# Kernel tuning notes

Hardware: AMD Instinct MI355X
Metric: run time of the kernel (lower is better)

## Reference

```python
import jax, jax.numpy as jnp
import numpy as np

L, C, H, DH, S, N, B = 12, 768, 12, 64, 2, 577, 1
ALT_START, ROPE_START = 0, 0
OUT_LAYERS = (2, 5, 8, 11)
EPS = 1e-6


def _ln(x, w, b):
    m = jnp.mean(x, axis=-1, keepdims=True)
    v = jnp.var(x, axis=-1, keepdims=True)
    return (x - m) * jax.lax.rsqrt(v + EPS) * w + b


def _rms(x, w):
    return x * jax.lax.rsqrt(jnp.mean(x * x, axis=-1, keepdims=True) + EPS) * w


def _rot_half(x):
    h = x.shape[-1] // 2
    return jnp.concatenate([-x[..., h:], x[..., :h]], axis=-1)


def _rope(t, cos, sin):
    # t: [Bf, H, N, DH]; cos/sin: [N, DH] split into y/x halves
    h = t.shape[-1] // 2
    tv, th = t[..., :h], t[..., h:]
    cy, cx = cos[..., :h], cos[..., h:]
    sy, sx = sin[..., :h], sin[..., h:]
    return jnp.concatenate([tv * cy + _rot_half(tv) * sy,
                            th * cx + _rot_half(th) * sx], axis=-1)


def _block(xf, cos, sin, kv, p):
    (qkv_w, qkv_b, qn, kn, pw, pb, g1, g2,
     n1w, n1b, n2w, n2b, f1w, f1b, f2w, f2b) = p
    Bf, Nn, Cc = xf.shape
    h = _ln(xf, n1w, n1b)
    qkv = (jnp.einsum('bnc,oc->bno', h, qkv_w) + qkv_b)
    qkv = qkv.reshape(Bf, Nn, 3, H, DH).transpose(2, 0, 3, 1, 4)
    q, k, v = qkv[0], qkv[1], qkv[2]
    q, k = _rms(q, qn), _rms(k, kn)
    q, k = _rope(q, cos, sin), _rope(k, cos, sin)
    bias = ((1.0 - kv) * (-10000.0))[:, None, None, :]
    scores = jnp.einsum('bhqd,bhkd->bhqk', q, k) / np.sqrt(DH) + bias
    attn = jax.nn.softmax(scores, axis=-1)
    o = jnp.einsum('bhqk,bhkd->bhqd', attn, v).transpose(0, 2, 1, 3).reshape(Bf, Nn, Cc)
    o = jnp.einsum('bnc,oc->bno', o, pw) + pb
    xf = xf + g1 * o
    h2 = _ln(xf, n2w, n2b)
    m = jax.nn.gelu(jnp.einsum('bnc,oc->bno', h2, f1w) + f1b, approximate=False)
    m = jnp.einsum('bnd,od->bno', m, f2w) + f2b
    return xf + g2 * m


def _forward(x, rope_cos_local, rope_sin_local, rope_cos_global, rope_sin_global,
             key_valid_local, key_valid_global, camera_token,
             qkv_w, qkv_b, q_norm_w, k_norm_w, proj_w, proj_b,
             ls1_gamma, ls2_gamma, norm1_w, norm1_b, norm2_w, norm2_b,
             fc1_w, fc1_b, fc2_w, fc2_b, final_norm_w, final_norm_b):
    Bb, Ss, Nn, Cc = x.shape
    stacked = (qkv_w, qkv_b, q_norm_w, k_norm_w, proj_w, proj_b, ls1_gamma,
               ls2_gamma, norm1_w, norm1_b, norm2_w, norm2_b, fc1_w, fc1_b,
               fc2_w, fc2_b)
    local_x = x
    outputs = []
    cam_token_out = None
    max_out = max(OUT_LAYERS)
    for i in range(L):
        if i == ALT_START:
            ref = jnp.broadcast_to(camera_token[:, :1], (Bb, 1, Cc))
            src = jnp.broadcast_to(camera_token[:, 1:], (Bb, Ss - 1, Cc))
            x = x.at[:, :, 0].set(jnp.concatenate([ref, src], axis=1))
        p = tuple(a[i] for a in stacked)
        is_global = (i % 2 == 1)  # alt_start == 0
        if is_global:
            xf = x.reshape(Bb, Ss * Nn, Cc)
            xf = _block(xf, rope_cos_global, rope_sin_global, key_valid_global, p)
            x = xf.reshape(Bb, Ss, Nn, Cc)
        else:
            xf = x.reshape(Bb * Ss, Nn, Cc)
            xf = _block(xf, rope_cos_local, rope_sin_local, key_valid_local, p)
            x = xf.reshape(Bb, Ss, Nn, Cc)
            local_x = x
        if i in OUT_LAYERS:
            out_x = jnp.concatenate([local_x, x], axis=-1)  # cat_token=True
            outputs.append(out_x)
            if i == max_out:
                cam_token_out = out_x[:, :, 0]
    processed = []
    for o in outputs:
        o = jnp.concatenate([o[..., :Cc], _ln(o[..., Cc:], final_norm_w, final_norm_b)], axis=-1)
        o = o[..., 1:, :]  # drop cam/cls token (num_register_tokens=0)
        processed.append(o)
    return (processed[0], processed[1], processed[2], processed[3], cam_token_out)


def setup_inputs() -> dict:
    key = jax.random.key(0)
    ks = iter(jax.random.split(key, 40))
    rn = lambda sh, s=0.02: jax.random.normal(next(ks), sh, dtype=jnp.float32) * s
    two_pi = 2.0 * np.pi
    ang_l = jax.random.uniform(next(ks), (N, DH), dtype=jnp.float32) * two_pi
    ang_g = jax.random.uniform(next(ks), (S * N, DH), dtype=jnp.float32) * two_pi
    kv_l = (jax.random.uniform(next(ks), (B * S, N)) > 0.1).astype(jnp.float32)
    kv_g = (jax.random.uniform(next(ks), (B, S * N)) > 0.1).astype(jnp.float32)
    return {
        'x': rn((B, S, N, C), 1.0),
        'rope_cos_local': jnp.cos(ang_l), 'rope_sin_local': jnp.sin(ang_l),
        'rope_cos_global': jnp.cos(ang_g), 'rope_sin_global': jnp.sin(ang_g),
        'key_valid_local': kv_l, 'key_valid_global': kv_g,
        'camera_token': rn((1, 2, C)),
        'qkv_w': rn((L, 3 * C, C)), 'qkv_b': rn((L, 3 * C)),
        'q_norm_w': jnp.ones((L, DH), jnp.float32),
        'k_norm_w': jnp.ones((L, DH), jnp.float32),
        'proj_w': rn((L, C, C)), 'proj_b': rn((L, C)),
        'ls1_gamma': rn((L, C), 0.1), 'ls2_gamma': rn((L, C), 0.1),
        'norm1_w': jnp.ones((L, C), jnp.float32), 'norm1_b': jnp.zeros((L, C), jnp.float32),
        'norm2_w': jnp.ones((L, C), jnp.float32), 'norm2_b': jnp.zeros((L, C), jnp.float32),
        'fc1_w': rn((L, 4 * C, C)), 'fc1_b': rn((L, 4 * C)),
        'fc2_w': rn((L, C, 4 * C)), 'fc2_b': rn((L, C)),
        'final_norm_w': jnp.ones((C,), jnp.float32),
        'final_norm_b': jnp.zeros((C,), jnp.float32),
    }


def reference(x, rope_cos_local, rope_sin_local, rope_cos_global, rope_sin_global,
              key_valid_local, key_valid_global, camera_token,
              qkv_w, qkv_b, q_norm_w, k_norm_w, proj_w, proj_b,
              ls1_gamma, ls2_gamma, norm1_w, norm1_b, norm2_w, norm2_b,
              fc1_w, fc1_b, fc2_w, fc2_b, final_norm_w, final_norm_b):
    return _forward(x, rope_cos_local, rope_sin_local, rope_cos_global, rope_sin_global,
                    key_valid_local, key_valid_global, camera_token,
                    qkv_w, qkv_b, q_norm_w, k_norm_w, proj_w, proj_b,
                    ls1_gamma, ls2_gamma, norm1_w, norm1_b, norm2_w, norm2_b,
                    fc1_w, fc1_b, fc2_w, fc2_b, final_norm_w, final_norm_b)
```

## Files before the change

kernel.cpp:

```cpp
#include <hip/hip_runtime.h>
#include <hip/hip_bf16.h>
#include <math.h>

typedef __hip_bfloat16 bf16;
typedef __attribute__((ext_vector_type(4))) float floatx4;
typedef __attribute__((ext_vector_type(8))) short shortx8;

#define T_TOK 1154
#define C_DIM 768
#define H_HEADS 12
#define NLOC 577
#define OUT_PER 1769472

#define NQ  1769472ull
#define NP  589824ull
#define NF1 2359296ull
#define NF2 2359296ull
#define NWTOT 7077888ull
#define WQ  0ull
#define WP  1769472ull
#define WF1 2359296ull
#define WF2 4718592ull

static __device__ __forceinline__ float b2f(bf16 v) { return __bfloat162float(v); }
static __device__ __forceinline__ bf16 f2b(float v) { return __float2bfloat16(v); }

static __device__ __forceinline__ void gload16(const bf16* g, short* l) {
    __builtin_amdgcn_global_load_lds(
        (__attribute__((address_space(1))) void*)(void*)g,
        (__attribute__((address_space(3))) void*)(void*)l, 16, 0, 0);
}

__global__ void k_init(const float* __restrict__ xin, const float* __restrict__ cam,
                       float* __restrict__ xF, int total) {
    int idx = blockIdx.x * 256 + threadIdx.x;
    if (idx >= total) return;
    int t = idx / C_DIM, c = idx - t * C_DIM;
    int s = t / NLOC, n = t - s * NLOC;
    float v = (n == 0) ? cam[s * C_DIM + c] : xin[idx];
    xF[idx] = v;
}

__global__ void k_cast(const float* __restrict__ src, bf16* __restrict__ dst, int total) {
    int idx = blockIdx.x * 256 + threadIdx.x;
    if (idx < total) dst[idx] = f2b(src[idx]);
}

__global__ __launch_bounds__(256) void k_wconv3(
    const float* __restrict__ wq, const float* __restrict__ wp,
    const float* __restrict__ wf1, const float* __restrict__ wf2,
    bf16* __restrict__ dst) {
    int typ = blockIdx.y, layer = blockIdx.z;
    size_t cnt, off;
    const float* srcb;
    if (typ == 0)      { cnt = NQ;  off = WQ;  srcb = wq; }
    else if (typ == 1) { cnt = NP;  off = WP;  srcb = wp; }
    else if (typ == 2) { cnt = NF1; off = WF1; srcb = wf1; }
    else               { cnt = NF2; off = WF2; srcb = wf2; }
    size_t e = ((size_t)blockIdx.x * 256 + threadIdx.x) * 8;
    if (e >= cnt) return;
    const float* src = srcb + (size_t)layer * cnt + e;
    bf16* d = dst + (size_t)layer * NWTOT + off + e;
    float4 a = *(const float4*)(src);
    float4 b = *(const float4*)(src + 4);
    bf16 pk[8];
    pk[0] = f2b(a.x); pk[1] = f2b(a.y); pk[2] = f2b(a.z); pk[3] = f2b(a.w);
    pk[4] = f2b(b.x); pk[5] = f2b(b.y); pk[6] = f2b(b.z); pk[7] = f2b(b.w);
    *(shortx8*)d = *(shortx8*)pk;
}

__global__ __launch_bounds__(256) void k_ln(const float* __restrict__ xF,
                                            const float* __restrict__ w, const float* __restrict__ b,
                                            bf16* __restrict__ out) {
    int t = blockIdx.x;
    const float* xr = xF + (size_t)t * C_DIM;
    float s = 0.f, s2 = 0.f;
    for (int c = threadIdx.x; c < C_DIM; c += 256) { float v = xr[c]; s += v; s2 += v * v; }
    __shared__ float red[8];
    for (int o = 32; o; o >>= 1) { s += __shfl_xor(s, o, 64); s2 += __shfl_xor(s2, o, 64); }
    int wv = threadIdx.x >> 6;
    if ((threadIdx.x & 63) == 0) { red[wv] = s; red[4 + wv] = s2; }
    __syncthreads();
    s = red[0] + red[1] + red[2] + red[3];
    s2 = red[4] + red[5] + red[6] + red[7];
    float mean = s * (1.0f / C_DIM);
    float var = s2 * (1.0f / C_DIM) - mean * mean;
    if (var < 0.f) var = 0.f;
    float inv = rsqrtf(var + 1e-6f);
    bf16* orow = out + (size_t)t * C_DIM;
    for (int c = threadIdx.x; c < C_DIM; c += 256) {
        float v = (xr[c] - mean) * inv * w[c] + b[c];
        orow[c] = f2b(v);
    }
}

template<int BM, int BN, int MODE>
__global__ __launch_bounds__(256) void k_gemmT(
    const bf16* __restrict__ A, const bf16* __restrict__ Bt,
    const float* __restrict__ bias, const float* __restrict__ gamma,
    bf16* __restrict__ outB, float* __restrict__ xio,
    int M, int N, int K, int mB, int kS) {
    constexpr int FM = BM / 32;
    constexpr int FN = BN / 32;
    __shared__ short At[2][BM * 64];
    __shared__ short Bs[2][BN * 64];
    int nwg = gridDim.x;
    int lid = blockIdx.x;
    int qd = nwg >> 3, rm = nwg & 7;
    int xcd = lid & 7, pos = lid >> 3;
    int lid2 = (xcd < rm ? xcd * (qd + 1) : rm * (qd + 1) + (xcd - rm) * qd) + pos;
    int mI = lid2 % mB;
    int rest = lid2 / mB;
    int nB = N / BN;
    int nI = rest % nB;
    int kI = rest / nB;
    int m0 = mI * BM, n0 = nI * BN;
    int Ksub = K / kS;
    int kOff = kI * Ksub;
    int tid = threadIdx.x;
    int w = tid >> 6, lane = tid & 63;
    int lr = lane & 15, lq = lane >> 4;
    int wm = w & 1, wn = w >> 1;
    int srow = tid >> 3;
    int schk = tid & 7;
    floatx4 acc[FM][FN] = {};

    auto stage = [&](int buf, int k0) {
        #pragma unroll
        for (int j = 0; j < BM / 32; j++) {
            int r = j * 32 + srow;
            int ar = m0 + r; if (ar >= M) ar = M - 1;
            int gs = schk ^ (r & 7);
            gload16(A + (size_t)ar * K + kOff + k0 + gs * 8, &At[buf][r * 64 + schk * 8]);
        }
        #pragma unroll
        for (int j = 0; j < BN / 32; j++) {
            int r = j * 32 + srow;
            int gs = schk ^ (r & 7);
            gload16(Bt + (size_t)(n0 + r) * K + kOff + k0 + gs * 8, &Bs[buf][r * 64 + schk * 8]);
        }
    };

    int nt = Ksub / 64;
    stage(0, 0);
    __syncthreads();
    int cur = 0;
    int rx = lr & 7;
    for (int t = 0; t < nt; ++t) {
        if (t + 1 < nt) stage(cur ^ 1, (t + 1) * 64);
        #pragma unroll
        for (int kk = 0; kk < 2; kk++) {
            shortx8 af[FM], bg[FN];
            #pragma unroll
            for (int mi = 0; mi < FM; mi++) {
                int rowl = wm * (BM / 2) + mi * 16 + lr;
                af[mi] = *(const shortx8*)&At[cur][rowl * 64 + ((kk * 4 + lq) ^ rx) * 8];
            }
            #pragma unroll
            for (int ni = 0; ni < FN; ni++) {
                int rowl = wn * (BN / 2) + ni * 16 + lr;
                bg[ni] = *(const shortx8*)&Bs[cur][rowl * 64 + ((kk * 4 + lq) ^ rx) * 8];
            }
            #pragma unroll
            for (int mi = 0; mi < FM; mi++)
                #pragma unroll
                for (int ni = 0; ni < FN; ni++)
                    acc[mi][ni] = __builtin_amdgcn_mfma_f32_16x16x32_bf16(af[mi], bg[ni], acc[mi][ni], 0, 0, 0);
        }
        __syncthreads();
        cur ^= 1;
    }

    #pragma unroll
    for (int mi = 0; mi < FM; mi++) {
        #pragma unroll
        for (int ni = 0; ni < FN; ni++) {
            int cc = n0 + wn * (BN / 2) + ni * 16 + lr;
            #pragma unroll
            for (int rg = 0; rg < 4; rg++) {
                int rr = m0 + wm * (BM / 2) + mi * 16 + lq * 4 + rg;
                if (rr < M) {
                    float u = acc[mi][ni][rg];
                    if (MODE == 2) {
                        u += (kI == 0) ? bias[cc] : 0.f;
                        float contrib = gamma[cc] * u;
                        if (kS > 1) atomicAdd(&xio[(size_t)rr * N + cc], contrib);
                        else        xio[(size_t)rr * N + cc] += contrib;
                    } else if (MODE == 1) {
                        u += bias[cc];
                        float g = 0.5f * u * (1.0f + erff(u * 0.70710678118f));
                        outB[(size_t)rr * N + cc] = f2b(g);
                    } else {
                        u += bias[cc];
                        outB[(size_t)rr * N + cc] = f2b(u);
                    }
                }
            }
        }
    }
}

__global__ __launch_bounds__(256) void k_gemmQKV(
    const bf16* __restrict__ A, const bf16* __restrict__ Bt,
    const float* __restrict__ bias,
    const float* __restrict__ qnw, const float* __restrict__ knw,
    const float* __restrict__ ctab, const float* __restrict__ stab, int posMod,
    bf16* __restrict__ qh, bf16* __restrict__ kh, bf16* __restrict__ vh,
    int M, int K) {
    constexpr int BM = 64, BN = 64, FM = 2, FN = 2;
    const int N = 2304, mB = 19;
    __shared__ short At[2][BM * 64];
    __shared__ short Bs[2][BN * 64];
    __shared__ float ssqS[2][64];
    int nwg = gridDim.x;
    int lid = blockIdx.x;
    int qd = nwg >> 3, rm = nwg & 7;
    int xcd = lid & 7, pos = lid >> 3;
    int lid2 = (xcd < rm ? xcd * (qd + 1) : rm * (qd + 1) + (xcd - rm) * qd) + pos;
    int mI = lid2 % mB;
    int nI = lid2 / mB;
    int m0 = mI * BM, n0 = nI * BN;
    int tid = threadIdx.x;
    int w = tid >> 6, lane = tid & 63;
    int lr = lane & 15, lq = lane >> 4;
    int wm = w & 1, wn = w >> 1;
    int srow = tid >> 3, schk = tid & 7;
    floatx4 acc[FM][FN] = {};

    auto stage = [&](int buf, int k0) {
        #pragma unroll
        for (int j = 0; j < BM / 32; j++) {
            int r = j * 32 + srow;
            int ar = m0 + r; if (ar >= M) ar = M - 1;
            int gs = schk ^ (r & 7);
            gload16(A + (size_t)ar * K + k0 + gs * 8, &At[buf][r * 64 + schk * 8]);
        }
        #pragma unroll
        for (int j = 0; j < BN / 32; j++) {
            int r = j * 32 + srow;
            int gs = schk ^ (r & 7);
            gload16(Bt + (size_t)(n0 + r) * K + k0 + gs * 8, &Bs[buf][r * 64 + schk * 8]);
        }
    };

    int nt = K / 64;
    stage(0, 0);
    __syncthreads();
    int cur = 0;
    int rx = lr & 7;
    for (int t = 0; t < nt; ++t) {
        if (t + 1 < nt) stage(cur ^ 1, (t + 1) * 64);
        #pragma unroll
        for (int kk = 0; kk < 2; kk++) {
            shortx8 af[FM], bg[FN];
            #pragma unroll
            for (int mi = 0; mi < FM; mi++) {
                int rowl = wm * 32 + mi * 16 + lr;
                af[mi] = *(const shortx8*)&At[cur][rowl * 64 + ((kk * 4 + lq) ^ rx) * 8];
            }
            #pragma unroll
            for (int ni = 0; ni < FN; ni++) {
                int rowl = wn * 32 + ni * 16 + lr;
                bg[ni] = *(const shortx8*)&Bs[cur][rowl * 64 + ((kk * 4 + lq) ^ rx) * 8];
            }
            #pragma unroll
            for (int mi = 0; mi < FM; mi++)
                #pragma unroll
                for (int ni = 0; ni < FN; ni++)
                    acc[mi][ni] = __builtin_amdgcn_mfma_f32_16x16x32_bf16(af[mi], bg[ni], acc[mi][ni], 0, 0, 0);
        }
        __syncthreads();
        cur ^= 1;
    }

    int tile6 = n0 >> 6;
    int typ = tile6 / 12;
    int hh = tile6 - typ * 12;
    float u[FM][FN][4];
    #pragma unroll
    for (int mi = 0; mi < FM; mi++)
        #pragma unroll
        for (int ni = 0; ni < FN; ni++) {
            int cc = n0 + wn * 32 + ni * 16 + lr;
            #pragma unroll
            for (int rg = 0; rg < 4; rg++) u[mi][ni][rg] = acc[mi][ni][rg] + bias[cc];
        }

    if (typ == 2) {
        #pragma unroll
        for (int mi = 0; mi < FM; mi++)
            #pragma unroll
            for (int rg = 0; rg < 4; rg++) {
                int rr = m0 + wm * 32 + mi * 16 + lq * 4 + rg;
                if (rr < M) {
                    #pragma unroll
                    for (int ni = 0; ni < FN; ni++) {
                        int d = wn * 32 + ni * 16 + lr;
                        vh[((size_t)hh * T_TOK + rr) * 64 + d] = f2b(u[mi][ni][rg]);
                    }
                }
            }
        return;
    }

    float sq[FM][4];
    #pragma unroll
    for (int mi = 0; mi < FM; mi++)
        #pragma unroll
        for (int rg = 0; rg < 4; rg++) {
            float s = u[mi][0][rg] * u[mi][0][rg] + u[mi][1][rg] * u[mi][1][rg];
            for (int o = 1; o < 16; o <<= 1) s += __shfl_xor(s, o, 16);
            sq[mi][rg] = s;
        }
    if (lr == 0) {
        #pragma unroll
        for (int mi = 0; mi < FM; mi++)
            #pragma unroll
            for (int rg = 0; rg < 4; rg++)
                ssqS[wn][wm * 32 + mi * 16 + lq * 4 + rg] = sq[mi][rg];
    }
    __syncthreads();
    const float* wt = (typ == 0) ? qnw : knw;
    bf16* dstp = (typ == 0) ? qh : kh;
    int d0 = wn * 32 + lr;
    int d1 = d0 + 16;
    float w0 = wt[d0], w1 = wt[d1];
    #pragma unroll
    for (int mi = 0; mi < FM; mi++) {
        #pragma unroll
        for (int rg = 0; rg < 4; rg++) {
            int rowl = wm * 32 + mi * 16 + lq * 4 + rg;
            int rr = m0 + rowl;
            if (rr >= M) continue;
            float ssq = ssqS[0][rowl] + ssqS[1][rowl];
            float rinv = rsqrtf(ssq * (1.0f / 64.0f) + 1e-6f);
            float n0v = u[mi][0][rg] * rinv * w0;
            float n1v = u[mi][1][rg] * rinv * w1;
            int p = (rr >= posMod) ? rr - posMod : rr;
            float c0 = ctab[p * 64 + d0], s0 = stab[p * 64 + d0];
            float c1 = ctab[p * 64 + d1], s1 = stab[p * 64 + d1];
            float o0 = n0v * c0 - n1v * s0;
            float o1 = n1v * c1 + n0v * s1;
            size_t ob = ((size_t)hh * T_TOK + rr) * 64;
            dstp[ob + d0] = f2b(o0);
            dstp[ob + d1] = f2b(o1);
        }
    }
}

__global__ __launch_bounds__(256) void k_attn2(
    const bf16* __restrict__ qh, const bf16* __restrict__ kh, const bf16* __restrict__ vh,
    const float* __restrict__ mask, bf16* __restrict__ out, int nk) {
    __shared__ short Ks[64 * 72];
    __shared__ short Vs[64 * 72];
    __shared__ short Ps[4][16 * 72];
    __shared__ float bias_s[64];
    int h = blockIdx.y;
    int base = blockIdx.z * nk;
    int tid = threadIdx.x;
    int wv = tid >> 6, lane = tid & 63;
    int lr = lane & 15, lq = lane >> 4;
    int q0 = blockIdx.x * 64 + wv * 16;
    shortx8 qf[2];
    {
        int qr = q0 + lr; if (qr >= nk) qr = nk - 1;
        const bf16* qp = qh + ((size_t)h * T_TOK + base + qr) * 64 + lq * 8;
        qf[0] = *(const shortx8*)(qp);
        qf[1] = *(const shortx8*)(qp + 32);
    }
    int kKr[2], kSeg[2], vKr[2], vSeg[2];
    #pragma unroll
    for (int c = 0; c < 2; c++) {
        int idx = tid + c * 256;
        kKr[c] = idx >> 3; kSeg[c] = idx & 7;
        vKr[c] = idx & 63; vSeg[c] = idx >> 6;
    }
    shortx8 kpre[2], vpre[2];
    float bpre = 0.f;
    auto prefetch = [&](int kbase) {
        #pragma unroll
        for (int c = 0; c < 2; c++) {
            int gk = kbase + kKr[c];
            shortx8 kv = {};
            if (gk < nk) kv = *(const shortx8*)(kh + ((size_t)h * T_TOK + base + gk) * 64 + kSeg[c] * 8);
            kpre[c] = kv;
            int gv = kbase + vKr[c];
            shortx8 vv = {};
            if (gv < nk) vv = *(const shortx8*)(vh + ((size_t)h * T_TOK + base + gv) * 64 + vSeg[c] * 8);
            vpre[c] = vv;
        }
        if (tid < 64) {
            int gk = kbase + tid;
            bpre = (gk < nk) ? (1.0f - mask[base + gk]) * -10000.0f : -30000.0f;
        }
    };
    float mrow[4] = {-3.0e38f, -3.0e38f, -3.0e38f, -3.0e38f};
    float lrow[4] = {0.f, 0.f, 0.f, 0.f};
    floatx4 accO[4] = {};
    short* pbuf = &Ps[wv][0];
    int nkt = (nk + 63) >> 6;
    prefetch(0);
    for (int kt0 = 0; kt0 < nkt; kt0++) {
        __syncthreads();
        #pragma unroll
        for (int c = 0; c < 2; c++) {
            *(shortx8*)&Ks[kKr[c] * 72 + kSeg[c] * 8] = kpre[c];
            bf16* vb = (bf16*)&vpre[c];
            #pragma unroll
            for (int j = 0; j < 8; j++)
                Vs[(vSeg[c] * 8 + j) * 72 + vKr[c]] = *(short*)&vb[j];
        }
        if (tid < 64) bias_s[tid] = bpre;
        if (kt0 + 1 < nkt) prefetch((kt0 + 1) * 64);
        __syncthreads();
        floatx4 s[4];
        #pragma unroll
        for (int nt = 0; nt < 4; nt++) {
            floatx4 accS = {};
            shortx8 k0 = *(const shortx8*)&Ks[(nt * 16 + lr) * 72 + lq * 8];
            shortx8 k1 = *(const shortx8*)&Ks[(nt * 16 + lr) * 72 + 32 + lq * 8];
            accS = __builtin_amdgcn_mfma_f32_16x16x32_bf16(qf[0], k0, accS, 0, 0, 0);
            accS = __builtin_amdgcn_mfma_f32_16x16x32_bf16(qf[1], k1, accS, 0, 0, 0);
            s[nt] = accS;
        }
        float tmax[4] = {-3.0e38f, -3.0e38f, -3.0e38f, -3.0e38f};
        #pragma unroll
        for (int nt = 0; nt < 4; nt++) {
            float bv = bias_s[nt * 16 + lr];
            #pragma unroll
            for (int rg = 0; rg < 4; rg++) {
                float sv = s[nt][rg] * 0.125f + bv;
                s[nt][rg] = sv;
                tmax[rg] = fmaxf(tmax[rg], sv);
            }
        }
        #pragma unroll
        for (int rg = 0; rg < 4; rg++) {
            for (int o = 1; o < 16; o <<= 1) tmax[rg] = fmaxf(tmax[rg], __shfl_xor(tmax[rg], o, 16));
        }
        float fac[4], tsum[4] = {0.f, 0.f, 0.f, 0.f};
        #pragma unroll
        for (int rg = 0; rg < 4; rg++) {
            float mn = fmaxf(mrow[rg], tmax[rg]);
            fac[rg] = __expf(mrow[rg] - mn);
            mrow[rg] = mn;
        }
        #pragma unroll
        for (int nt = 0; nt < 4; nt++) {
            #pragma unroll
            for (int rg = 0; rg < 4; rg++) {
                float e = __expf(s[nt][rg] - mrow[rg]);
                s[nt][rg] = e;
                tsum[rg] += e;
            }
        }
        #pragma unroll
        for (int rg = 0; rg < 4; rg++) {
            for (int o = 1; o < 16; o <<= 1) tsum[rg] += __shfl_xor(tsum[rg], o, 16);
            lrow[rg] = lrow[rg] * fac[rg] + tsum[rg];
        }
        #pragma unroll
        for (int dt = 0; dt < 4; dt++)
            #pragma unroll
            for (int rg = 0; rg < 4; rg++) accO[dt][rg] *= fac[rg];
        #pragma unroll
        for (int nt = 0; nt < 4; nt++) {
            #pragma unroll
            for (int rg = 0; rg < 4; rg++) {
                bf16 pv = f2b(s[nt][rg]);
                pbuf[(lq * 4 + rg) * 72 + nt * 16 + lr] = *(short*)&pv;
            }
        }
        #pragma unroll
        for (int ks = 0; ks < 2; ks++) {
            shortx8 pf = *(const shortx8*)&pbuf[lr * 72 + ks * 32 + lq * 8];
            #pragma unroll
            for (int dt = 0; dt < 4; dt++) {
                shortx8 vf = *(const shortx8*)&Vs[(dt * 16 + lr) * 72 + ks * 32 + lq * 8];
                accO[dt] = __builtin_amdgcn_mfma_f32_16x16x32_bf16(pf, vf, accO[dt], 0, 0, 0);
            }
        }
    }
    float invl[4];
    #pragma unroll
    for (int rg = 0; rg < 4; rg++) invl[rg] = 1.0f / lrow[rg];
    #pragma unroll
    for (int rg = 0; rg < 4; rg++) {
        int qr = q0 + lq * 4 + rg;
        if (qr < nk) {
            bf16* orow = out + (size_t)(base + qr) * C_DIM + h * 64 + lr;
            #pragma unroll
            for (int dt = 0; dt < 4; dt++)
                orow[dt * 16] = f2b(accO[dt][rg] * invl[rg]);
        }
    }
}

__global__ __launch_bounds__(256) void k_output(
    const float* __restrict__ xF, const bf16* __restrict__ lxB,
    const float* __restrict__ fw, const float* __restrict__ fb, float* __restrict__ dst) {
    int b = blockIdx.x;
    int s = b / 576, nn = b - s * 576;
    int t = s * NLOC + nn + 1;
    const float* xr = xF + (size_t)t * C_DIM;
    float sum = 0.f, s2 = 0.f;
    for (int c = threadIdx.x; c < C_DIM; c += 256) { float v = xr[c]; sum += v; s2 += v * v; }
    __shared__ float red[8];
    for (int o = 32; o; o >>= 1) { sum += __shfl_xor(sum, o, 64); s2 += __shfl_xor(s2, o, 64); }
    if ((threadIdx.x & 63) == 0) { red[threadIdx.x >> 6] = sum; red[4 + (threadIdx.x >> 6)] = s2; }
    __syncthreads();
    sum = red[0] + red[1] + red[2] + red[3];
    s2 = red[4] + red[5] + red[6] + red[7];
    float mean = sum * (1.0f / C_DIM);
    float var = s2 * (1.0f / C_DIM) - mean * mean;
    if (var < 0.f) var = 0.f;
    float inv = rsqrtf(var + 1e-6f);
    float* orow = dst + (size_t)b * 1536;
    const bf16* lr = lxB + (size_t)t * C_DIM;
    for (int c = threadIdx.x; c < C_DIM; c += 256) {
        orow[c] = b2f(lr[c]);
        float v = (xr[c] - mean) * inv * fw[c] + fb[c];
        orow[768 + c] = v;
    }
}

__global__ void k_cam(const float* __restrict__ xF, const bf16* __restrict__ lxB,
                      float* __restrict__ dst) {
    for (int idx = threadIdx.x; idx < 2 * 1536; idx += 256) {
        int s = idx / 1536, c = idx - s * 1536;
        int t = s * NLOC;
        float v = (c < 768) ? b2f(lxB[(size_t)t * 768 + c]) : xF[(size_t)t * 768 + (c - 768)];
        dst[idx] = v;
    }
}

extern "C" void kernel_launch(void* const* d_in, const int* in_sizes, int n_in,
                              void* d_out, int out_size, void* d_ws, size_t ws_size,
                              hipStream_t stream) {
    const float* xin  = (const float*)d_in[0];
    const float* rcl  = (const float*)d_in[1];
    const float* rsl  = (const float*)d_in[2];
    const float* rcg  = (const float*)d_in[3];
    const float* rsg  = (const float*)d_in[4];
    const float* kvl  = (const float*)d_in[5];
    const float* kvg  = (const float*)d_in[6];
    const float* cam  = (const float*)d_in[7];
    const float* qkvw = (const float*)d_in[8];
    const float* qkvb = (const float*)d_in[9];
    const float* qnw  = (const float*)d_in[10];
    const float* knw  = (const float*)d_in[11];
    const float* pw   = (const float*)d_in[12];
    const float* pb   = (const float*)d_in[13];
    const float* ls1  = (const float*)d_in[14];
    const float* ls2  = (const float*)d_in[15];
    const float* n1w  = (const float*)d_in[16];
    const float* n1b  = (const float*)d_in[17];
    const float* n2w  = (const float*)d_in[18];
    const float* n2b  = (const float*)d_in[19];
    const float* f1w  = (const float*)d_in[20];
    const float* f1b  = (const float*)d_in[21];
    const float* f2w  = (const float*)d_in[22];
    const float* f2b_ = (const float*)d_in[23];
    const float* fnw  = (const float*)d_in[24];
    const float* fnb  = (const float*)d_in[25];

    char* ws = (char*)d_ws;
    const size_t TC = (size_t)T_TOK * C_DIM;
    float* xF  = (float*)ws; ws += TC * 4;
    bf16* bufA = (bf16*)ws;  ws += (size_t)T_TOK * 3072 * 2;
    bf16* qhb  = (bf16*)ws;  ws += TC * 2;
    bf16* khb  = (bf16*)ws;  ws += TC * 2;
    bf16* vhb  = (bf16*)ws;  ws += TC * 2;
    bf16* hbuf = (bf16*)ws;  ws += TC * 2;
    bf16* lxB  = (bf16*)ws;  ws += TC * 2;
    bf16* wAll = (bf16*)ws;
    size_t usedBase = (size_t)(ws - (char*)d_ws);
    bool bigW = ws_size >= usedBase + 12ull * NWTOT * 2ull;
    (void)n_in; (void)in_sizes; (void)out_size;

    float* out_b = (float*)d_out;

    k_init<<<(int)((TC + 255) / 256), 256, 0, stream>>>(xin, cam, xF, (int)TC);
    if (bigW)
        k_wconv3<<<dim3(1152, 4, 12), 256, 0, stream>>>(qkvw, pw, f1w, f2w, wAll);

    int outIdx = 0;
    for (int i = 0; i < 12; i++) {
        bool isGlobal = (i & 1);
        bf16* wL;
        if (bigW) {
            wL = wAll + (size_t)i * NWTOT;
        } else {
            k_wconv3<<<dim3(1152, 4, 1), 256, 0, stream>>>(
                qkvw + (size_t)i * NQ, pw + (size_t)i * NP,
                f1w + (size_t)i * NF1, f2w + (size_t)i * NF2, wAll);
            wL = wAll;
        }
        k_ln<<<T_TOK, 256, 0, stream>>>(xF, n1w + (size_t)i * 768, n1b + (size_t)i * 768, hbuf);
        k_gemmQKV<<<684, 256, 0, stream>>>(hbuf, wL + WQ,
            qkvb + (size_t)i * 2304,
            qnw + (size_t)i * 64, knw + (size_t)i * 64,
            isGlobal ? rcg : rcl, isGlobal ? rsg : rsl, isGlobal ? 1154 : 577,
            qhb, khb, vhb, T_TOK, 768);
        if (isGlobal)
            k_attn2<<<dim3(19, 12, 1), 256, 0, stream>>>(qhb, khb, vhb, kvg, hbuf, 1154);
        else
            k_attn2<<<dim3(10, 12, 2), 256, 0, stream>>>(qhb, khb, vhb, kvl, hbuf, 577);
        k_gemmT<64, 64, 2><<<456, 256, 0, stream>>>(hbuf, wL + WP,
            pb + (size_t)i * 768, ls1 + (size_t)i * 768, nullptr, xF, T_TOK, 768, 768, 19, 2);
        k_ln<<<T_TOK, 256, 0, stream>>>(xF, n2w + (size_t)i * 768, n2b + (size_t)i * 768, hbuf);
        k_gemmT<64, 64, 1><<<912, 256, 0, stream>>>(hbuf, wL + WF1,
            f1b + (size_t)i * 3072, nullptr, bufA, nullptr, T_TOK, 3072, 768, 19, 1);
        k_gemmT<64, 64, 2><<<912, 256, 0, stream>>>(bufA, wL + WF2,
            f2b_ + (size_t)i * 768, ls2 + (size_t)i * 768, nullptr, xF, T_TOK, 768, 3072, 19, 4);

        if (i == 2 || i == 4 || i == 8 || i == 10)
            k_cast<<<(int)((TC + 255) / 256), 256, 0, stream>>>(xF, lxB, (int)TC);

        if (i == 2 || i == 5 || i == 8 || i == 11) {
            k_output<<<1152, 256, 0, stream>>>(xF, lxB, fnw, fnb, out_b + (size_t)outIdx * OUT_PER);
            if (i == 11)
                k_cam<<<1, 256, 0, stream>>>(xF, lxB, out_b + 4ull * OUT_PER);
            outIdx++;
        }
    }
}
```

Before: 1.783 ms.

## Replace atomic split-K residual adds with partial buffers folded into layernorm

The proj and FC2 GEMMs now write their split-K partials into a two-slice float buffer instead of doing atomicAdd or read-modify-write into the residual. The next layernorm, or a new fold kernel at output layers, adds the partials into the residual stream and can also cast it to bf16. FC2 split-K drops from four slices to two, halving its grid. The weight conversion kernel also handles 16 elements per thread. This removes atomic traffic at the cost of extra partial-buffer reads and writes and a less parallel FC2.

```diff
diff --git a/kernel.cpp b/kernel.cpp
--- a/kernel.cpp
+++ b/kernel.cpp
@@ -41,9 +41,21 @@
     xF[idx] = v;
 }
 
-__global__ void k_cast(const float* __restrict__ src, bf16* __restrict__ dst, int total) {
-    int idx = blockIdx.x * 256 + threadIdx.x;
-    if (idx < total) dst[idx] = f2b(src[idx]);
+__global__ __launch_bounds__(256) void k_fold(
+    float* __restrict__ xF, const float* __restrict__ p0, const float* __restrict__ p1,
+    bf16* __restrict__ lxB, int doCast, int total4) {
+    int i = blockIdx.x * 256 + threadIdx.x;
+    if (i >= total4) return;
+    float4 x = ((float4*)xF)[i];
+    float4 a = ((const float4*)p0)[i];
+    float4 b = ((const float4*)p1)[i];
+    x.x += a.x + b.x; x.y += a.y + b.y; x.z += a.z + b.z; x.w += a.w + b.w;
+    ((float4*)xF)[i] = x;
+    if (doCast) {
+        bf16 pk[4];
+        pk[0] = f2b(x.x); pk[1] = f2b(x.y); pk[2] = f2b(x.z); pk[3] = f2b(x.w);
+        *(short4*)(lxB + (size_t)i * 4) = *(short4*)pk;
+    }
 }
 
 __global__ __launch_bounds__(256) void k_wconv3(
@@ -57,26 +69,39 @@
     else if (typ == 1) { cnt = NP;  off = WP;  srcb = wp; }
     else if (typ == 2) { cnt = NF1; off = WF1; srcb = wf1; }
     else               { cnt = NF2; off = WF2; srcb = wf2; }
-    size_t e = ((size_t)blockIdx.x * 256 + threadIdx.x) * 8;
+    size_t e = ((size_t)blockIdx.x * 256 + threadIdx.x) * 16;
     if (e >= cnt) return;
     const float* src = srcb + (size_t)layer * cnt + e;
     bf16* d = dst + (size_t)layer * NWTOT + off + e;
-    float4 a = *(const float4*)(src);
-    float4 b = *(const float4*)(src + 4);
-    bf16 pk[8];
-    pk[0] = f2b(a.x); pk[1] = f2b(a.y); pk[2] = f2b(a.z); pk[3] = f2b(a.w);
-    pk[4] = f2b(b.x); pk[5] = f2b(b.y); pk[6] = f2b(b.z); pk[7] = f2b(b.w);
-    *(shortx8*)d = *(shortx8*)pk;
-}
-
-__global__ __launch_bounds__(256) void k_ln(const float* __restrict__ xF,
-                                            const float* __restrict__ w, const float* __restrict__ b,
-                                            bf16* __restrict__ out) {
+    #pragma unroll
+    for (int h = 0; h < 2; h++) {
+        float4 a = *(const float4*)(src + h * 8);
+        float4 b = *(const float4*)(src + h * 8 + 4);
+        bf16 pk[8];
+        pk[0] = f2b(a.x); pk[1] = f2b(a.y); pk[2] = f2b(a.z); pk[3] = f2b(a.w);
+        pk[4] = f2b(b.x); pk[5] = f2b(b.y); pk[6] = f2b(b.z); pk[7] = f2b(b.w);
+        *(shortx8*)(d + h * 8) = *(shortx8*)pk;
+    }
+}
+
+__global__ __launch_bounds__(256) void k_ln(
+    float* __restrict__ xF, const float* __restrict__ p0, const float* __restrict__ p1,
+    const float* __restrict__ w, const float* __restrict__ b,
+    bf16* __restrict__ out, int fold) {
+    __shared__ float rowS[C_DIM];
+    __shared__ float red[8];
     int t = blockIdx.x;
-    const float* xr = xF + (size_t)t * C_DIM;
+    float* xr = xF + (size_t)t * C_DIM;
     float s = 0.f, s2 = 0.f;
-    for (int c = threadIdx.x; c < C_DIM; c += 256) { float v = xr[c]; s += v; s2 += v * v; }
-    __shared__ float red[8];
+    for (int c = threadIdx.x; c < C_DIM; c += 256) {
+        float v = xr[c];
+        if (fold) {
+            v += p0[(size_t)t * C_DIM + c] + p1[(size_t)t * C_DIM + c];
+            xr[c] = v;
+        }
+        rowS[c] = v;
+        s += v; s2 += v * v;
+    }
     for (int o = 32; o; o >>= 1) { s += __shfl_xor(s, o, 64); s2 += __shfl_xor(s2, o, 64); }
     int wv = threadIdx.x >> 6;
     if ((threadIdx.x & 63) == 0) { red[wv] = s; red[4 + wv] = s2; }
@@ -89,7 +114,7 @@
     float inv = rsqrtf(var + 1e-6f);
     bf16* orow = out + (size_t)t * C_DIM;
     for (int c = threadIdx.x; c < C_DIM; c += 256) {
-        float v = (xr[c] - mean) * inv * w[c] + b[c];
+        float v = (rowS[c] - mean) * inv * w[c] + b[c];
         orow[c] = f2b(v);
     }
 }
@@ -181,11 +206,9 @@
                 int rr = m0 + wm * (BM / 2) + mi * 16 + lq * 4 + rg;
                 if (rr < M) {
                     float u = acc[mi][ni][rg];
-                    if (MODE == 2) {
+                    if (MODE == 4) {
                         u += (kI == 0) ? bias[cc] : 0.f;
-                        float contrib = gamma[cc] * u;
-                        if (kS > 1) atomicAdd(&xio[(size_t)rr * N + cc], contrib);
-                        else        xio[(size_t)rr * N + cc] += contrib;
+                        xio[(size_t)kI * ((size_t)M * N) + (size_t)rr * N + cc] = gamma[cc] * u;
                     } else if (MODE == 1) {
                         u += bias[cc];
                         float g = 0.5f * u * (1.0f + erff(u * 0.70710678118f));
@@ -208,7 +231,7 @@
     bf16* __restrict__ qh, bf16* __restrict__ kh, bf16* __restrict__ vh,
     int M, int K) {
     constexpr int BM = 64, BN = 64, FM = 2, FN = 2;
-    const int N = 2304, mB = 19;
+    const int mB = 19;
     __shared__ short At[2][BM * 64];
     __shared__ short Bs[2][BN * 64];
     __shared__ float ssqS[2][64];
@@ -573,16 +596,20 @@
     bf16* vhb  = (bf16*)ws;  ws += TC * 2;
     bf16* hbuf = (bf16*)ws;  ws += TC * 2;
     bf16* lxB  = (bf16*)ws;  ws += TC * 2;
+    float* PP  = (float*)ws; ws += TC * 4 * 2;
     bf16* wAll = (bf16*)ws;
     size_t usedBase = (size_t)(ws - (char*)d_ws);
     bool bigW = ws_size >= usedBase + 12ull * NWTOT * 2ull;
     (void)n_in; (void)in_sizes; (void)out_size;
 
     float* out_b = (float*)d_out;
+    const int TC4 = (int)(TC / 4);
 
     k_init<<<(int)((TC + 255) / 256), 256, 0, stream>>>(xin, cam, xF, (int)TC);
     if (bigW)
-        k_wconv3<<<dim3(1152, 4, 12), 256, 0, stream>>>(qkvw, pw, f1w, f2w, wAll);
+        k_wconv3<<<dim3(576, 4, 12), 256, 0, stream>>>(qkvw, pw, f1w, f2w, wAll);
+
+    auto foldAfter = [](int i) { return i == 2 || i == 4 || i == 5 || i == 8 || i == 10 || i == 11; };
 
     int outIdx = 0;
     for (int i = 0; i < 12; i++) {
@@ -591,12 +618,14 @@
         if (bigW) {
             wL = wAll + (size_t)i * NWTOT;
         } else {
-            k_wconv3<<<dim3(1152, 4, 1), 256, 0, stream>>>(
+            k_wconv3<<<dim3(576, 4, 1), 256, 0, stream>>>(
                 qkvw + (size_t)i * NQ, pw + (size_t)i * NP,
                 f1w + (size_t)i * NF1, f2w + (size_t)i * NF2, wAll);
             wL = wAll;
         }
-        k_ln<<<T_TOK, 256, 0, stream>>>(xF, n1w + (size_t)i * 768, n1b + (size_t)i * 768, hbuf);
+        int ln1Fold = (i > 0 && !foldAfter(i - 1)) ? 1 : 0;
+        k_ln<<<T_TOK, 256, 0, stream>>>(xF, PP, PP + TC,
+            n1w + (size_t)i * 768, n1b + (size_t)i * 768, hbuf, ln1Fold);
         k_gemmQKV<<<684, 256, 0, stream>>>(hbuf, wL + WQ,
             qkvb + (size_t)i * 2304,
             qnw + (size_t)i * 64, knw + (size_t)i * 64,
@@ -606,16 +635,19 @@
             k_attn2<<<dim3(19, 12, 1), 256, 0, stream>>>(qhb, khb, vhb, kvg, hbuf, 1154);
         else
             k_attn2<<<dim3(10, 12, 2), 256, 0, stream>>>(qhb, khb, vhb, kvl, hbuf, 577);
-        k_gemmT<64, 64, 2><<<456, 256, 0, stream>>>(hbuf, wL + WP,
-            pb + (size_t)i * 768, ls1 + (size_t)i * 768, nullptr, xF, T_TOK, 768, 768, 19, 2);
-        k_ln<<<T_TOK, 256, 0, stream>>>(xF, n2w + (size_t)i * 768, n2b + (size_t)i * 768, hbuf);
+        k_gemmT<64, 64, 4><<<456, 256, 0, stream>>>(hbuf, wL + WP,
+            pb + (size_t)i * 768, ls1 + (size_t)i * 768, nullptr, PP, T_TOK, 768, 768, 19, 2);
+        k_ln<<<T_TOK, 256, 0, stream>>>(xF, PP, PP + TC,
+            n2w + (size_t)i * 768, n2b + (size_t)i * 768, hbuf, 1);
         k_gemmT<64, 64, 1><<<912, 256, 0, stream>>>(hbuf, wL + WF1,
             f1b + (size_t)i * 3072, nullptr, bufA, nullptr, T_TOK, 3072, 768, 19, 1);
-        k_gemmT<64, 64, 2><<<912, 256, 0, stream>>>(bufA, wL + WF2,
-            f2b_ + (size_t)i * 768, ls2 + (size_t)i * 768, nullptr, xF, T_TOK, 768, 3072, 19, 4);
-
-        if (i == 2 || i == 4 || i == 8 || i == 10)
-            k_cast<<<(int)((TC + 255) / 256), 256, 0, stream>>>(xF, lxB, (int)TC);
+        k_gemmT<64, 64, 4><<<456, 256, 0, stream>>>(bufA, wL + WF2,
+            f2b_ + (size_t)i * 768, ls2 + (size_t)i * 768, nullptr, PP, T_TOK, 768, 3072, 19, 2);
+
+        if (foldAfter(i)) {
+            int doCast = (i == 2 || i == 4 || i == 8 || i == 10) ? 1 : 0;
+            k_fold<<<(TC4 + 255) / 256, 256, 0, stream>>>(xF, PP, PP + TC, lxB, doCast, TC4);
+        }
 
         if (i == 2 || i == 5 || i == 8 || i == 11) {
             k_output<<<1152, 256, 0, stream>>>(xF, lxB, fnw, fnb, out_b + (size_t)outIdx * OUT_PER);
```

Result: no change. 1.775 ms (-0.4%).
